# Performance work log

Hardware: AMD Instinct MI355X
Metric: run time of the kernel (lower is better)

## Reference

```python
import jax, jax.numpy as jnp
from jax import lax
import numpy as np

H = 8  # hidden size


def setup_inputs() -> dict:
    key = jax.random.key(0)
    ks = jax.random.split(key, 7)
    B, T, I = 8192, 512, 1
    return {
        "x": jax.random.normal(ks[0], (B, T, I), dtype=jnp.float32),
        "W_ih": jax.random.normal(ks[1], (3 * H, I), dtype=jnp.float32) * 0.3,
        "W_hh": jax.random.normal(ks[2], (3 * H, H), dtype=jnp.float32) * 0.3,
        "b_ih": jax.random.normal(ks[3], (3 * H,), dtype=jnp.float32) * 0.1,
        "b_hh": jax.random.normal(ks[4], (3 * H,), dtype=jnp.float32) * 0.1,
        "W_fc": jax.random.normal(ks[5], (1, H), dtype=jnp.float32) * 0.3,
        "b_fc": jax.random.normal(ks[6], (1,), dtype=jnp.float32) * 0.1,
    }


def _gru_seq(x, W_ih, W_hh, b_ih, b_hh):
    # x: [B, T, I] -> output: [B, T, H]. PyTorch gate order: r, z, n.
    B = x.shape[0]
    # Precompute input-to-gate projections for all timesteps at once.
    xg = jnp.einsum("bti,gi->btg", x, W_ih) + b_ih  # [B, T, 3H]
    xg = jnp.moveaxis(xg, 1, 0)  # [T, B, 3H]

    def step(h, xt):
        hg = h @ W_hh.T + b_hh  # [B, 3H]
        xr, xz, xn = jnp.split(xt, 3, axis=-1)
        hr, hz, hn = jnp.split(hg, 3, axis=-1)
        r = jax.nn.sigmoid(xr + hr)
        z = jax.nn.sigmoid(xz + hz)
        n = jnp.tanh(xn + r * hn)
        h_new = (1.0 - z) * n + z * h
        return h_new, h_new

    h0 = jnp.zeros((B, H), dtype=x.dtype)
    _, hs = lax.scan(step, h0, xg)  # hs: [T, B, H]
    return jnp.moveaxis(hs, 0, 1)  # [B, T, H]


def reference(x, W_ih, W_hh, b_ih, b_hh, W_fc, b_fc):
    out = _gru_seq(x, W_ih, W_hh, b_ih, b_hh)  # [B, T, H]
    y_hat = out @ W_fc.T + b_fc  # [B, T, 1]
    return y_hat
```

## Files before the change

kernel.cpp:

```cpp
#include <hip/hip_runtime.h>

#define T_LEN 512
#define LOG2E 1.44269504f

#define DPP_XOR1 0xB1
#define DPP_XOR2 0x4E
#define DPP_XOR3 0x1B
#define DPP_XOR8 0x128

#define DPPF(v, ctrl)                                                      \
  __int_as_float(__builtin_amdgcn_update_dpp(0, __float_as_int(v), (ctrl), \
                                             0xF, 0xF, true))

#define STEP(i, xi)                                                        \
  do {                                                                     \
    const float a0 = h;                                                    \
    const float a1 = DPPF(h, DPP_XOR1);                        \
    const float a2 = DPPF(h, DPP_XOR2);                        \
    const float a3 = DPPF(h, DPP_XOR3);                        \
    const float a4 = DPPF(a0, DPP_XOR8);                       \
    const float a5 = DPPF(a1, DPP_XOR8);                       \
    const float a6 = DPPF(a2, DPP_XOR8);                       \
    const float a7 = DPPF(a3, DPP_XOR8);                       \
                     \
    float tr = __builtin_fmaf(xi, wi_r, c_r);                              \
    tr = __builtin_fmaf(wr0, a0, tr);                                      \
    tr = __builtin_fmaf(wr1, a1, tr);                                      \
    tr = __builtin_fmaf(wr2, a2, tr);                                      \
    tr = __builtin_fmaf(wr3, a3, tr);                                      \
    float ur = wr4 * a4;                                                   \
    ur = __builtin_fmaf(wr5, a5, ur);                                      \
    ur = __builtin_fmaf(wr6, a6, ur);                                      \
    ur = __builtin_fmaf(wr7, a7, ur);                                      \
                                                               \
    float tz = __builtin_fmaf(xi, wi_z, c_z);                              \
    tz = __builtin_fmaf(wz0, a0, tz);                                      \
    tz = __builtin_fmaf(wz1, a1, tz);                                      \
    tz = __builtin_fmaf(wz2, a2, tz);                                      \
    tz = __builtin_fmaf(wz3, a3, tz);                                      \
    float uz = wz4 * a4;                                                   \
    uz = __builtin_fmaf(wz5, a5, uz);                                      \
    uz = __builtin_fmaf(wz6, a6, uz);                                      \
    uz = __builtin_fmaf(wz7, a7, uz);                                      \
                            \
    float tn = __builtin_fmaf(wn0, a0, c_n);                               \
    tn = __builtin_fmaf(wn1, a1, tn);                                      \
    tn = __builtin_fmaf(wn2, a2, tn);                                      \
    tn = __builtin_fmaf(wn3, a3, tn);                                      \
    float un = wn4 * a4;                                                   \
    un = __builtin_fmaf(wn5, a5, un);                                      \
    un = __builtin_fmaf(wn6, a6, un);                                      \
    un = __builtin_fmaf(wn7, a7, un);                                      \
    const float r =                                                        \
        __builtin_amdgcn_rcpf(1.0f + __builtin_amdgcn_exp2f(tr + ur));     \
    const float z =                                                        \
        __builtin_amdgcn_rcpf(1.0f + __builtin_amdgcn_exp2f(tz + uz));     \
    const float xn = __builtin_fmaf(xi, wi_n, bi_n);                       \
    const float pn = __builtin_fmaf(r, tn + un, xn);                       \
    const float uu =                                                       \
        __builtin_amdgcn_rcpf(1.0f + __builtin_amdgcn_exp2f(pn));          \
    const float nn = __builtin_fmaf(-2.0f, uu, 1.0f);            \
    h = __builtin_fmaf(z, a0 - nn, nn);              \
       \
    float m = __builtin_fmaf(h, wfc, bfc8);                                \
    m += DPPF(m, DPP_XOR1);                                                \
    m += DPPF(m, DPP_XOR2);                                                \
    m += DPPF(m, DPP_XOR8);                                                \
    ysel = is_##i ? m : ysel;                                              \
  } while (0)

__global__ void __launch_bounds__(256) gru_fused(
    const float* __restrict__ x, const float* __restrict__ W_ih,
    const float* __restrict__ W_hh, const float* __restrict__ b_ih,
    const float* __restrict__ b_hh, const float* __restrict__ W_fc,
    const float* __restrict__ b_fc, float* __restrict__ out) {
  const int tid = blockIdx.x * blockDim.x + threadIdx.x;
  const int pos = tid & 3;
  const int grp = (tid >> 2) & 1;
  const int hlf = (tid >> 3) & 1;
  const int j = pos | (hlf << 2);
  const int b = ((tid >> 4) << 1) | grp;

  const float* wr = W_hh + j * 8;
  const float* wz = W_hh + (8 + j) * 8;
  const float* wn = W_hh + (16 + j) * 8;
  const float SN = -LOG2E, SP = 2.0f * LOG2E;
  const float wr0 = SN * wr[j ^ 0], wr1 = SN * wr[j ^ 1];
  const float wr2 = SN * wr[j ^ 2], wr3 = SN * wr[j ^ 3];
  const float wr4 = SN * wr[j ^ 4], wr5 = SN * wr[j ^ 5];
  const float wr6 = SN * wr[j ^ 6], wr7 = SN * wr[j ^ 7];
  const float wz0 = SN * wz[j ^ 0], wz1 = SN * wz[j ^ 1];
  const float wz2 = SN * wz[j ^ 2], wz3 = SN * wz[j ^ 3];
  const float wz4 = SN * wz[j ^ 4], wz5 = SN * wz[j ^ 5];
  const float wz6 = SN * wz[j ^ 6], wz7 = SN * wz[j ^ 7];
  const float wn0 = SP * wn[j ^ 0], wn1 = SP * wn[j ^ 1];
  const float wn2 = SP * wn[j ^ 2], wn3 = SP * wn[j ^ 3];
  const float wn4 = SP * wn[j ^ 4], wn5 = SP * wn[j ^ 5];
  const float wn6 = SP * wn[j ^ 6], wn7 = SP * wn[j ^ 7];

  const float c_r = SN * (b_ih[j] + b_hh[j]);
  const float c_z = SN * (b_ih[8 + j] + b_hh[8 + j]);
  const float c_n = SP * b_hh[16 + j];
  const float bi_n = SP * b_ih[16 + j];
  const float wi_r = SN * W_ih[j], wi_z = SN * W_ih[8 + j],
              wi_n = SP * W_ih[16 + j];
  const float wfc = W_fc[j];
  const float bfc8 = b_fc[0] * 0.125f;

  const bool is_0 = (j == 0), is_1 = (j == 1), is_2 = (j == 2),
             is_3 = (j == 3);
  const bool is_4 = (j == 4), is_5 = (j == 5), is_6 = (j == 6),
             is_7 = (j == 7);

  const float* xp = x + (size_t)b * T_LEN;
  float* op = out + (size_t)b * T_LEN;

  float h = 0.0f;
  const float4* xq = reinterpret_cast<const float4*>(xp);
  float4 cA = xq[0], cB = xq[1];
  for (int t0 = 0; t0 < T_LEN; t0 += 8) {
    float4 nA, nB;
    if (t0 + 8 < T_LEN) {
      nA = xq[(t0 >> 2) + 2];
      nB = xq[(t0 >> 2) + 3];
    } else {
      nA = cA;
      nB = cB;
    }
    float ysel = 0.0f;
    STEP(0, cA.x);
    STEP(1, cA.y);
    STEP(2, cA.z);
    STEP(3, cA.w);
    STEP(4, cB.x);
    STEP(5, cB.y);
    STEP(6, cB.z);
    STEP(7, cB.w);
    op[t0 + j] = ysel;
    cA = nA;
    cB = nB;
  }
}

extern "C" void kernel_launch(void* const* d_in, const int* in_sizes, int n_in,
                              void* d_out, int out_size, void* d_ws,
                              size_t ws_size, hipStream_t stream) {
  const float* x = (const float*)d_in[0];
  const float* W_ih = (const float*)d_in[1];
  const float* W_hh = (const float*)d_in[2];
  const float* b_ih = (const float*)d_in[3];
  const float* b_hh = (const float*)d_in[4];
  const float* W_fc = (const float*)d_in[5];
  const float* b_fc = (const float*)d_in[6];
  float* out = (float*)d_out;

  const int B = in_sizes[0] / T_LEN;
  const int threads = B * 8;
  gru_fused<<<threads / 256, 256, 0, stream>>>(x, W_ih, W_hh, b_ih, b_hh, W_fc,
                                               b_fc, out);
}
```

Before: 62.10 us.

## Use packed fp16 dot2 for recurrent matvec with fewer DPP shuffles

Converts the hidden state and recurrent weights to packed half2 and computes the 8-wide recurrent dot products with v_dot2_f32_f16. This halves the FMA count per gate and cuts the DPP permutes from seven to four per step. It also reorders the final update so z*h and 1-z are computed earlier. The cost is reduced precision in the recurrent matvec (fp16 rtz for h and the weights), which could accumulate error over 512 timesteps.

Measured after the change: 59.84 us. 1.04x faster.

```diff
diff --git a/kernel.cpp b/kernel.cpp
--- a/kernel.cpp
+++ b/kernel.cpp
@@ -1,4 +1,6 @@
 #include <hip/hip_runtime.h>
+
+typedef __fp16 f16x2 __attribute__((ext_vector_type(2)));
 
 #define T_LEN 512
 #define LOG2E 1.44269504f
@@ -8,65 +10,53 @@
 #define DPP_XOR3 0x1B
 #define DPP_XOR8 0x128
 
-#define DPPF(v, ctrl)                                                      \
-  __int_as_float(__builtin_amdgcn_update_dpp(0, __float_as_int(v), (ctrl), \
-                                             0xF, 0xF, true))
+#define DPPI(v, ctrl) __builtin_amdgcn_update_dpp(0, (v), (ctrl), 0xF, 0xF, true)
+#define DPPF(v, ctrl) __int_as_float(DPPI(__float_as_int(v), (ctrl)))
+#define DPPH2(v, ctrl) \
+  __builtin_bit_cast(f16x2, DPPI(__builtin_bit_cast(int, (v)), (ctrl)))
 
-#define STEP(i, xi)                                                        \
-  do {                                                                     \
-    const float a0 = h;                                                    \
-    const float a1 = DPPF(h, DPP_XOR1);                        \
-    const float a2 = DPPF(h, DPP_XOR2);                        \
-    const float a3 = DPPF(h, DPP_XOR3);                        \
-    const float a4 = DPPF(a0, DPP_XOR8);                       \
-    const float a5 = DPPF(a1, DPP_XOR8);                       \
-    const float a6 = DPPF(a2, DPP_XOR8);                       \
-    const float a7 = DPPF(a3, DPP_XOR8);                       \
-                     \
-    float tr = __builtin_fmaf(xi, wi_r, c_r);                              \
-    tr = __builtin_fmaf(wr0, a0, tr);                                      \
-    tr = __builtin_fmaf(wr1, a1, tr);                                      \
-    tr = __builtin_fmaf(wr2, a2, tr);                                      \
-    tr = __builtin_fmaf(wr3, a3, tr);                                      \
-    float ur = wr4 * a4;                                                   \
-    ur = __builtin_fmaf(wr5, a5, ur);                                      \
-    ur = __builtin_fmaf(wr6, a6, ur);                                      \
-    ur = __builtin_fmaf(wr7, a7, ur);                                      \
-                                                               \
-    float tz = __builtin_fmaf(xi, wi_z, c_z);                              \
-    tz = __builtin_fmaf(wz0, a0, tz);                                      \
-    tz = __builtin_fmaf(wz1, a1, tz);                                      \
-    tz = __builtin_fmaf(wz2, a2, tz);                                      \
-    tz = __builtin_fmaf(wz3, a3, tz);                                      \
-    float uz = wz4 * a4;                                                   \
-    uz = __builtin_fmaf(wz5, a5, uz);                                      \
-    uz = __builtin_fmaf(wz6, a6, uz);                                      \
-    uz = __builtin_fmaf(wz7, a7, uz);                                      \
-                            \
-    float tn = __builtin_fmaf(wn0, a0, c_n);                               \
-    tn = __builtin_fmaf(wn1, a1, tn);                                      \
-    tn = __builtin_fmaf(wn2, a2, tn);                                      \
-    tn = __builtin_fmaf(wn3, a3, tn);                                      \
-    float un = wn4 * a4;                                                   \
-    un = __builtin_fmaf(wn5, a5, un);                                      \
-    un = __builtin_fmaf(wn6, a6, un);                                      \
-    un = __builtin_fmaf(wn7, a7, un);                                      \
-    const float r =                                                        \
-        __builtin_amdgcn_rcpf(1.0f + __builtin_amdgcn_exp2f(tr + ur));     \
-    const float z =                                                        \
-        __builtin_amdgcn_rcpf(1.0f + __builtin_amdgcn_exp2f(tz + uz));     \
-    const float xn = __builtin_fmaf(xi, wi_n, bi_n);                       \
-    const float pn = __builtin_fmaf(r, tn + un, xn);                       \
-    const float uu =                                                       \
-        __builtin_amdgcn_rcpf(1.0f + __builtin_amdgcn_exp2f(pn));          \
-    const float nn = __builtin_fmaf(-2.0f, uu, 1.0f);            \
-    h = __builtin_fmaf(z, a0 - nn, nn);              \
-       \
-    float m = __builtin_fmaf(h, wfc, bfc8);                                \
-    m += DPPF(m, DPP_XOR1);                                                \
-    m += DPPF(m, DPP_XOR2);                                                \
-    m += DPPF(m, DPP_XOR8);                                                \
-    ysel = is_##i ? m : ysel;                                              \
+#define FDOT2(a, b, c) __builtin_amdgcn_fdot2((a), (b), (c), false)
+
+#define STEP(i, xi)                                                         \
+  do {                                                                      \
+          \
+    const f16x2 p01 = __builtin_amdgcn_cvt_pkrtz(h, DPPF(h, DPP_XOR1));     \
+    const f16x2 p45 = DPPH2(p01, DPP_XOR8);            \
+    const f16x2 p23 = DPPH2(p01, DPP_XOR2);            \
+    const f16x2 p67 = DPPH2(p45, DPP_XOR2);            \
+                                       \
+    float rA = FDOT2(p01, wr0, __builtin_fmaf(xi, wi_r, c_r));              \
+    rA = FDOT2(p23, wr1, rA);                                               \
+    float rB = FDOT2(p45, wr2, 0.0f);                                       \
+    rB = FDOT2(p67, wr3, rB);                                               \
+                                                                \
+    float zA = FDOT2(p01, wz0, __builtin_fmaf(xi, wi_z, c_z));              \
+    zA = FDOT2(p23, wz1, zA);                                               \
+    float zB = FDOT2(p45, wz2, 0.0f);                                       \
+    zB = FDOT2(p67, wz3, zB);                                               \
+                                                     \
+    float nA = FDOT2(p01, wn0, c_n);                                        \
+    nA = FDOT2(p23, wn1, nA);                                               \
+    float nB = FDOT2(p45, wn2, 0.0f);                                       \
+    nB = FDOT2(p67, wn3, nB);                                               \
+    const float r =                                                         \
+        __builtin_amdgcn_rcpf(1.0f + __builtin_amdgcn_exp2f(rA + rB));      \
+    const float z =                                                         \
+        __builtin_amdgcn_rcpf(1.0f + __builtin_amdgcn_exp2f(zA + zB));      \
+    const float omz = 1.0f - z;                  \
+    const float zh = z * h;                      \
+    const float xn = __builtin_fmaf(xi, wi_n, bi_n);                        \
+    const float pn = __builtin_fmaf(r, nA + nB, xn);                        \
+    const float uu =                                                        \
+        __builtin_amdgcn_rcpf(1.0f + __builtin_amdgcn_exp2f(pn));           \
+    const float nn = __builtin_fmaf(-2.0f, uu, 1.0f);             \
+    h = __builtin_fmaf(omz, nn, zh);                \
+                          \
+    float m = __builtin_fmaf(h, wfc, bfc8);                                 \
+    m += DPPF(m, DPP_XOR1);                                                 \
+    m += DPPF(m, DPP_XOR2);                                                 \
+    m += DPPF(m, DPP_XOR8);                                                 \
+    ysel = is_##i ? m : ysel;                                               \
   } while (0)
 
 __global__ void __launch_bounds__(256) gru_fused(
@@ -85,18 +75,18 @@
   const float* wz = W_hh + (8 + j) * 8;
   const float* wn = W_hh + (16 + j) * 8;
   const float SN = -LOG2E, SP = 2.0f * LOG2E;
-  const float wr0 = SN * wr[j ^ 0], wr1 = SN * wr[j ^ 1];
-  const float wr2 = SN * wr[j ^ 2], wr3 = SN * wr[j ^ 3];
-  const float wr4 = SN * wr[j ^ 4], wr5 = SN * wr[j ^ 5];
-  const float wr6 = SN * wr[j ^ 6], wr7 = SN * wr[j ^ 7];
-  const float wz0 = SN * wz[j ^ 0], wz1 = SN * wz[j ^ 1];
-  const float wz2 = SN * wz[j ^ 2], wz3 = SN * wz[j ^ 3];
-  const float wz4 = SN * wz[j ^ 4], wz5 = SN * wz[j ^ 5];
-  const float wz6 = SN * wz[j ^ 6], wz7 = SN * wz[j ^ 7];
-  const float wn0 = SP * wn[j ^ 0], wn1 = SP * wn[j ^ 1];
-  const float wn2 = SP * wn[j ^ 2], wn3 = SP * wn[j ^ 3];
-  const float wn4 = SP * wn[j ^ 4], wn5 = SP * wn[j ^ 5];
-  const float wn6 = SP * wn[j ^ 6], wn7 = SP * wn[j ^ 7];
+  const f16x2 wr0 = __builtin_amdgcn_cvt_pkrtz(SN * wr[j ^ 0], SN * wr[j ^ 1]);
+  const f16x2 wr1 = __builtin_amdgcn_cvt_pkrtz(SN * wr[j ^ 2], SN * wr[j ^ 3]);
+  const f16x2 wr2 = __builtin_amdgcn_cvt_pkrtz(SN * wr[j ^ 4], SN * wr[j ^ 5]);
+  const f16x2 wr3 = __builtin_amdgcn_cvt_pkrtz(SN * wr[j ^ 6], SN * wr[j ^ 7]);
+  const f16x2 wz0 = __builtin_amdgcn_cvt_pkrtz(SN * wz[j ^ 0], SN * wz[j ^ 1]);
+  const f16x2 wz1 = __builtin_amdgcn_cvt_pkrtz(SN * wz[j ^ 2], SN * wz[j ^ 3]);
+  const f16x2 wz2 = __builtin_amdgcn_cvt_pkrtz(SN * wz[j ^ 4], SN * wz[j ^ 5]);
+  const f16x2 wz3 = __builtin_amdgcn_cvt_pkrtz(SN * wz[j ^ 6], SN * wz[j ^ 7]);
+  const f16x2 wn0 = __builtin_amdgcn_cvt_pkrtz(SP * wn[j ^ 0], SP * wn[j ^ 1]);
+  const f16x2 wn1 = __builtin_amdgcn_cvt_pkrtz(SP * wn[j ^ 2], SP * wn[j ^ 3]);
+  const f16x2 wn2 = __builtin_amdgcn_cvt_pkrtz(SP * wn[j ^ 4], SP * wn[j ^ 5]);
+  const f16x2 wn3 = __builtin_amdgcn_cvt_pkrtz(SP * wn[j ^ 6], SP * wn[j ^ 7]);
 
   const float c_r = SN * (b_ih[j] + b_hh[j]);
   const float c_z = SN * (b_ih[8 + j] + b_hh[8 + j]);
@@ -119,13 +109,13 @@
   const float4* xq = reinterpret_cast<const float4*>(xp);
   float4 cA = xq[0], cB = xq[1];
   for (int t0 = 0; t0 < T_LEN; t0 += 8) {
-    float4 nA, nB;
+    float4 nA4, nB4;
     if (t0 + 8 < T_LEN) {
-      nA = xq[(t0 >> 2) + 2];
-      nB = xq[(t0 >> 2) + 3];
+      nA4 = xq[(t0 >> 2) + 2];
+      nB4 = xq[(t0 >> 2) + 3];
     } else {
-      nA = cA;
-      nB = cB;
+      nA4 = cA;
+      nB4 = cB;
     }
     float ysel = 0.0f;
     STEP(0, cA.x);
@@ -137,8 +127,8 @@
     STEP(6, cB.z);
     STEP(7, cB.w);
     op[t0 + j] = ysel;
-    cA = nA;
-    cB = nB;
+    cA = nA4;
+    cB = nB4;
   }
 }
 
```
